# Kernel tuning notes

Hardware: AMD Instinct MI355X
Metric: run time of the kernel (lower is better)

The kernel has to match this reference:

```python
import jax, jax.numpy as jnp
import numpy as np

HEADS = 16
HEAD_DIM = 64
TOKEN_DIM = 1024
INNER = HEADS * HEAD_DIM


def setup_inputs() -> dict:
    key = jax.random.key(0)
    k1, k2, k3, k4 = jax.random.split(key, 4)
    x = jax.random.normal(k1, (2, 2048, TOKEN_DIM), dtype=jnp.float32)
    # nn.Linear(token_dim, inner*3, bias=False): weight [3*inner, token_dim]
    w_qkv = jax.random.normal(k2, (3 * INNER, TOKEN_DIM), dtype=jnp.float32) * (TOKEN_DIM ** -0.5)
    # nn.Linear(inner, token_dim): weight [token_dim, inner], bias [token_dim]
    w_out = jax.random.normal(k3, (TOKEN_DIM, INNER), dtype=jnp.float32) * (INNER ** -0.5)
    b_out = jax.random.normal(k4, (TOKEN_DIM,), dtype=jnp.float32) * 0.01
    return {"x": x, "w_qkv": w_qkv, "w_out": w_out, "b_out": b_out}


def reference(x, w_qkv, w_out, b_out):
    b, n, _ = x.shape
    scale = HEAD_DIM ** -0.5
    qkv = x @ w_qkv.T                                  # [b, n, 3*inner]
    q, k, v = jnp.split(qkv, 3, axis=-1)
    def split_heads(t):
        return t.reshape(b, n, HEADS, HEAD_DIM).transpose(0, 2, 1, 3)  # [b,h,n,d]
    q, k, v = split_heads(q), split_heads(k), split_heads(v)
    dot = jnp.einsum('bhtd,bhsd->bhts', q, k) * scale  # [b,h,n,n]
    attn = jax.nn.softmax(dot, axis=-1)
    out = jnp.einsum('bhts,bhsd->bhtd', attn, v)       # [b,h,n,d]
    out = out.transpose(0, 2, 1, 3).reshape(b, n, INNER)
    return out @ w_out.T + b_out
```

## Files before the change

kernel.cpp:

```cpp
#include <hip/hip_runtime.h>
#include <hip/hip_bf16.h>

typedef short short4v __attribute__((ext_vector_type(4)));
typedef short short8 __attribute__((ext_vector_type(8)));
typedef float float4v __attribute__((ext_vector_type(4)));

#define HEADS 16
#define HDIM 64
#define TOKDIM 1024
#define SEQ 2048
#define BATCH 2
#define BH (BATCH*HEADS)
#define MROWS (BATCH*SEQ)

__device__ __forceinline__ short f2b(float f) {
    __hip_bfloat16 h = __float2bfloat16(f);
    return *reinterpret_cast<short*>(&h);
}
__device__ __forceinline__ float b2f(short s) {
    __hip_bfloat16 h;
    *reinterpret_cast<short*>(&h) = s;
    return __bfloat162float(h);
}
__device__ __forceinline__ int pack2(float a, float b) {
    return (((int)f2b(b)) << 16) | (((int)f2b(a)) & 0xffff);
}

__device__ __forceinline__ short8 load8_f32_bf16(const float* __restrict__ p) {
    float4v a = *(const float4v*)p;
    float4v b = *(const float4v*)(p + 4);
    short8 r;
    r[0]=f2b(a[0]); r[1]=f2b(a[1]); r[2]=f2b(a[2]); r[3]=f2b(a[3]);
    r[4]=f2b(b[0]); r[5]=f2b(b[1]); r[6]=f2b(b[2]); r[7]=f2b(b[3]);
    return r;
}

#define BM 128
#define BN 128
#define BK 32
#define LDT 40

__global__ __launch_bounds__(256)
void gemm_qkv(const float* __restrict__ A, const float* __restrict__ W,
              short* __restrict__ Qo, short* __restrict__ Ko, short* __restrict__ Vto)
{
    __shared__ __align__(16) short As[BM*LDT];
    __shared__ __align__(16) short Bs[BN*LDT];
    const int tid  = threadIdx.x;
    const int lane = tid & 63;
    const int wave = tid >> 6;
    const int wm = wave >> 1, wn = wave & 1;
    const int m0 = blockIdx.x * BM;
    const int n0 = blockIdx.y * BN;
    const int col16 = lane & 15, quad = lane >> 4;
    const int Kdim = TOKDIM;

    float4v acc[4][4];
    #pragma unroll
    for (int i=0;i<4;i++)
        #pragma unroll
        for (int j=0;j<4;j++) acc[i][j] = (float4v){0.f,0.f,0.f,0.f};

    for (int k0 = 0; k0 < Kdim; k0 += BK) {
        __syncthreads();
        #pragma unroll
        for (int s = 0; s < 2; ++s) {
            int blk = tid + s*256;
            int r  = blk >> 2;
            int kb = blk & 3;
            *(short8*)&As[r*LDT + kb*8] = load8_f32_bf16(&A[(size_t)(m0 + r)*Kdim + k0 + kb*8]);
            *(short8*)&Bs[r*LDT + kb*8] = load8_f32_bf16(&W[(size_t)(n0 + r)*Kdim + k0 + kb*8]);
        }
        __syncthreads();
        short8 af[4], bfr[4];
        #pragma unroll
        for (int i=0;i<4;i++) af[i]  = *(const short8*)&As[(wm*64 + i*16 + col16)*LDT + quad*8];
        #pragma unroll
        for (int j=0;j<4;j++) bfr[j] = *(const short8*)&Bs[(wn*64 + j*16 + col16)*LDT + quad*8];
        #pragma unroll
        for (int i=0;i<4;i++)
            #pragma unroll
            for (int j=0;j<4;j++)
                acc[i][j] = __builtin_amdgcn_mfma_f32_16x16x32_bf16(af[i], bfr[j], acc[i][j], 0,0,0);
    }

    #pragma unroll
    for (int i=0;i<4;i++)
        #pragma unroll
        for (int j=0;j<4;j++) {
            const int n = n0 + wn*64 + j*16 + col16;
            const int part = n >> 10;
            const int h = (n & 1023) >> 6;
            const int d = n & 63;
            const int mb = m0 + wm*64 + i*16 + quad*4;
            const int b = mb >> 11;
            const int t = mb & 2047;
            if (part == 2) {
                union { short4v s; int2 i2; } w;
                #pragma unroll
                for (int r=0;r<4;r++) w.s[r] = f2b(acc[i][j][r]);
                *(int2*)&Vto[((size_t)(b*HEADS + h)*HDIM + d)*SEQ + t] = w.i2;
            } else {
                short* dst = (part == 0) ? Qo : Ko;
                #pragma unroll
                for (int r=0;r<4;r++)
                    dst[((size_t)(b*HEADS + h)*SEQ + t + r)*HDIM + d] = f2b(acc[i][j][r]);
            }
        }
}

__global__ __launch_bounds__(256)
void gemm_out(const short* __restrict__ A, const float* __restrict__ W,
              const float* __restrict__ bias, float* __restrict__ C)
{
    __shared__ __align__(16) short As[BM*LDT];
    __shared__ __align__(16) short Bs[BN*LDT];
    const int tid  = threadIdx.x;
    const int lane = tid & 63;
    const int wave = tid >> 6;
    const int wm = wave >> 1, wn = wave & 1;
    const int m0 = blockIdx.x * BM;
    const int n0 = blockIdx.y * BN;
    const int col16 = lane & 15, quad = lane >> 4;
    const int Kdim = TOKDIM, Ncols = TOKDIM;

    float4v acc[4][4];
    #pragma unroll
    for (int i=0;i<4;i++)
        #pragma unroll
        for (int j=0;j<4;j++) acc[i][j] = (float4v){0.f,0.f,0.f,0.f};

    for (int k0 = 0; k0 < Kdim; k0 += BK) {
        __syncthreads();
        #pragma unroll
        for (int s = 0; s < 2; ++s) {
            int blk = tid + s*256;
            int r  = blk >> 2;
            int kb = blk & 3;
            *(short8*)&As[r*LDT + kb*8] = *(const short8*)&A[(size_t)(m0 + r)*Kdim + k0 + kb*8];
            *(short8*)&Bs[r*LDT + kb*8] = load8_f32_bf16(&W[(size_t)(n0 + r)*Kdim + k0 + kb*8]);
        }
        __syncthreads();
        short8 af[4], bfr[4];
        #pragma unroll
        for (int i=0;i<4;i++) af[i]  = *(const short8*)&As[(wm*64 + i*16 + col16)*LDT + quad*8];
        #pragma unroll
        for (int j=0;j<4;j++) bfr[j] = *(const short8*)&Bs[(wn*64 + j*16 + col16)*LDT + quad*8];
        #pragma unroll
        for (int i=0;i<4;i++)
            #pragma unroll
            for (int j=0;j<4;j++)
                acc[i][j] = __builtin_amdgcn_mfma_f32_16x16x32_bf16(af[i], bfr[j], acc[i][j], 0,0,0);
    }

    #pragma unroll
    for (int i=0;i<4;i++)
        #pragma unroll
        for (int j=0;j<4;j++) {
            const int n = n0 + wn*64 + j*16 + col16;
            #pragma unroll
            for (int r=0;r<4;r++) {
                const int m = m0 + wm*64 + i*16 + quad*4 + r;
                C[(size_t)m*Ncols + n] = acc[i][j][r] + bias[n];
            }
        }
}

#define AQB 128
#define KT  64
#define VLD 72

__global__ __launch_bounds__(256, 4)
void attn_kernel(const short* __restrict__ Q, const short* __restrict__ K,
                 const short* __restrict__ Vt, short* __restrict__ AO)
{
    __shared__ __align__(16) short Ks[2][KT*VLD];
    __shared__ __align__(16) short Vs[2][HDIM*VLD];

    const int tid   = threadIdx.x;
    const int lane  = tid & 63;
    const int wave  = tid >> 6;
    const int col16 = lane & 15, quad = lane >> 4;
    const int bh = blockIdx.y;
    const int qb = blockIdx.x*AQB + wave*32;

    const short* Qb = Q  + (size_t)bh*SEQ*HDIM;
    const short* Kb = K  + (size_t)bh*SEQ*HDIM;
    const short* Vb = Vt + (size_t)bh*HDIM*SEQ;

    const int sr = tid >> 2;
    const int sc = (tid & 3) * 16;
    const int rho = sr & 31;
    const int kslot = (sr & 32) + ((rho & 4) << 2) + ((rho & 24) >> 1) + (rho & 3);

    short8 qf[2][2];
    #pragma unroll
    for (int qg=0; qg<2; ++qg)
        #pragma unroll
        for (int kh=0; kh<2; ++kh) {
            short8 raw = *(const short8*)&Qb[(size_t)(qb+qg*16+col16)*HDIM + kh*32 + quad*8];
            #pragma unroll
            for (int j=0;j<8;++j) raw[j] = f2b(b2f(raw[j]) * 0.125f);
            qf[qg][kh] = raw;
        }

    float4v o[2][4];
    #pragma unroll
    for (int qg=0;qg<2;qg++)
        #pragma unroll
        for (int dt=0;dt<4;dt++) o[qg][dt] = (float4v){0.f,0.f,0.f,0.f};
    float lsum[2] = {0.f, 0.f};

    {
        short8 k0 = *(const short8*)&Kb[(size_t)sr*HDIM + sc];
        short8 k1 = *(const short8*)&Kb[(size_t)sr*HDIM + sc + 8];
        short8 v0 = *(const short8*)&Vb[(size_t)sr*SEQ + sc];
        short8 v1 = *(const short8*)&Vb[(size_t)sr*SEQ + sc + 8];
        *(short8*)&Ks[0][kslot*VLD + sc]     = k0;
        *(short8*)&Ks[0][kslot*VLD + sc + 8] = k1;
        *(short8*)&Vs[0][sr*VLD + sc]        = v0;
        *(short8*)&Vs[0][sr*VLD + sc + 8]    = v1;
    }
    __syncthreads();

    const int NT = SEQ / KT;
    for (int tile = 0; tile < NT; ++tile) {
        const int buf = tile & 1;

        short8 nk0, nk1, nv0, nv1;
        const bool more = (tile + 1 < NT);
        if (more) {
            const int s1 = (tile + 1) * KT;
            nk0 = *(const short8*)&Kb[(size_t)(s1 + sr)*HDIM + sc];
            nk1 = *(const short8*)&Kb[(size_t)(s1 + sr)*HDIM + sc + 8];
            nv0 = *(const short8*)&Vb[(size_t)sr*SEQ + s1 + sc];
            nv1 = *(const short8*)&Vb[(size_t)sr*SEQ + s1 + sc + 8];
        }

        #pragma unroll
        for (int kk = 0; kk < 2; ++kk) {
            short8 ka[2][2];
            #pragma unroll
            for (int nt=0; nt<2; ++nt)
                #pragma unroll
                for (int kh=0; kh<2; ++kh)
                    ka[nt][kh] = *(const short8*)&Ks[buf][(kk*32 + nt*16 + col16)*VLD + kh*32 + quad*8];
            short8 va[4];
            #pragma unroll
            for (int dt=0; dt<4; ++dt)
                va[dt] = *(const short8*)&Vs[buf][(dt*16 + col16)*VLD + kk*32 + quad*8];

            #pragma unroll
            for (int qg=0; qg<2; ++qg) {
                float4v st[2];
                #pragma unroll
                for (int nt=0; nt<2; ++nt) {
                    float4v z = (float4v){0.f,0.f,0.f,0.f};
                    z = __builtin_amdgcn_mfma_f32_16x16x32_bf16(ka[nt][0], qf[qg][0], z, 0,0,0);
                    z = __builtin_amdgcn_mfma_f32_16x16x32_bf16(ka[nt][1], qf[qg][1], z, 0,0,0);
                    st[nt] = z;
                }
                union { int i[4]; short8 s8; } pb;
                float p00 = __expf(st[0][0]), p01 = __expf(st[0][1]);
                float p02 = __expf(st[0][2]), p03 = __expf(st[0][3]);
                float p10 = __expf(st[1][0]), p11 = __expf(st[1][1]);
                float p12 = __expf(st[1][2]), p13 = __expf(st[1][3]);
                lsum[qg] += ((p00+p01) + (p02+p03)) + ((p10+p11) + (p12+p13));
                pb.i[0] = pack2(p00, p01); pb.i[1] = pack2(p02, p03);
                pb.i[2] = pack2(p10, p11); pb.i[3] = pack2(p12, p13);

                #pragma unroll
                for (int dt=0; dt<4; ++dt)
                    o[qg][dt] = __builtin_amdgcn_mfma_f32_16x16x32_bf16(va[dt], pb.s8, o[qg][dt], 0,0,0);
            }
        }

        if (more) {
            const int nb = buf ^ 1;
            *(short8*)&Ks[nb][kslot*VLD + sc]     = nk0;
            *(short8*)&Ks[nb][kslot*VLD + sc + 8] = nk1;
            *(short8*)&Vs[nb][sr*VLD + sc]        = nv0;
            *(short8*)&Vs[nb][sr*VLD + sc + 8]    = nv1;
        }
        __syncthreads();
    }

    #pragma unroll
    for (int qg=0; qg<2; ++qg) {
        lsum[qg] += __shfl_xor(lsum[qg], 16);
        lsum[qg] += __shfl_xor(lsum[qg], 32);
    }

    const int b = bh >> 4, h = bh & 15;
    #pragma unroll
    for (int qg=0; qg<2; ++qg) {
        const float inv = 1.0f / lsum[qg];
        const int t = qb + qg*16 + col16;
        #pragma unroll
        for (int dt=0; dt<4; ++dt) {
            union { short4v s; int2 i2; } w;
            #pragma unroll
            for (int r=0;r<4;++r) w.s[r] = f2b(o[qg][dt][r] * inv);
            *(int2*)&AO[((size_t)(b*SEQ + t))*TOKDIM + h*64 + dt*16 + quad*4] = w.i2;
        }
    }
}

extern "C" void kernel_launch(void* const* d_in, const int* in_sizes, int n_in,
                              void* d_out, int out_size, void* d_ws, size_t ws_size,
                              hipStream_t stream)
{
    const float* x    = (const float*)d_in[0];
    const float* wqkv = (const float*)d_in[1];
    const float* wout = (const float*)d_in[2];
    const float* bout = (const float*)d_in[3];
    float* out = (float*)d_out;

    char* ws = (char*)d_ws;
    const size_t SZ = (size_t)BH*SEQ*HDIM*sizeof(short);
    short* Qt = (short*)(ws);
    short* Kt = (short*)(ws + SZ);
    short* AO = (short*)(ws + 2*SZ);
    short* Vt = (short*)(ws + 3*SZ);

    gemm_qkv<<<dim3(MROWS/BM, (3*TOKDIM)/BN), 256, 0, stream>>>(x, wqkv, Qt, Kt, Vt);
    attn_kernel<<<dim3(SEQ/AQB, BH), 256, 0, stream>>>(Qt, Kt, Vt, AO);
    gemm_out<<<dim3(MROWS/BM, TOKDIM/BN), 256, 0, stream>>>(AO, wout, bout, out);
}
```

Baseline: 201.3 us.

## Pre-convert inputs to bf16 and stage GEMM tiles via direct global-to-LDS loads

Adds a conversion kernel that turns x, w_qkv and w_out into bf16 once per call. The QKV and output GEMMs can then stage tiles with global_load_lds straight into unpadded shared memory, instead of each block re-reading and converting fp32 tiles through registers. The output GEMM tile is reduced to 64 rows, which doubles its block count, and the bias load is hoisted out of the store loop. The trade-off is an extra launch and extra memory traffic for the conversion, plus possible LDS bank conflicts because the padding was removed.

```diff
diff --git a/kernel.cpp b/kernel.cpp
--- a/kernel.cpp
+++ b/kernel.cpp
@@ -25,7 +25,6 @@
 __device__ __forceinline__ int pack2(float a, float b) {
     return (((int)f2b(b)) << 16) | (((int)f2b(a)) & 0xffff);
 }
-
 __device__ __forceinline__ short8 load8_f32_bf16(const float* __restrict__ p) {
     float4v a = *(const float4v*)p;
     float4v b = *(const float4v*)(p + 4);
@@ -35,25 +34,42 @@
     return r;
 }
 
-#define BM 128
-#define BN 128
-#define BK 32
-#define LDT 40
+__device__ __forceinline__ void stage16(const void* g, void* l) {
+    __builtin_amdgcn_global_load_lds((const __attribute__((address_space(1))) void*)g,
+                                     (__attribute__((address_space(3))) void*)l, 16, 0, 0);
+}
 
 __global__ __launch_bounds__(256)
-void gemm_qkv(const float* __restrict__ A, const float* __restrict__ W,
+void cvt_bf16(const float* __restrict__ x,  short* __restrict__ xb,  int n8x,
+              const float* __restrict__ wq, short* __restrict__ wqb, int n8q,
+              const float* __restrict__ wo, short* __restrict__ wob, int n8o)
+{
+    int i = blockIdx.x*256 + threadIdx.x;
+    const float* s; short* d; int off;
+    if (i < n8x)                  { s = x;  d = xb;  off = i; }
+    else if (i < n8x + n8q)       { s = wq; d = wqb; off = i - n8x; }
+    else if (i < n8x + n8q + n8o) { s = wo; d = wob; off = i - n8x - n8q; }
+    else return;
+    *(short8*)&d[(size_t)off*8] = load8_f32_bf16(&s[(size_t)off*8]);
+}
+
+template<int ABF16>
+__global__ __launch_bounds__(256)
+void gemm_qkv(const void* __restrict__ Ap, const short* __restrict__ Wq,
               short* __restrict__ Qo, short* __restrict__ Ko, short* __restrict__ Vto)
 {
-    __shared__ __align__(16) short As[BM*LDT];
-    __shared__ __align__(16) short Bs[BN*LDT];
+    __shared__ __align__(16) short As[128*32];
+    __shared__ __align__(16) short Bs[128*32];
     const int tid  = threadIdx.x;
     const int lane = tid & 63;
     const int wave = tid >> 6;
     const int wm = wave >> 1, wn = wave & 1;
-    const int m0 = blockIdx.x * BM;
-    const int n0 = blockIdx.y * BN;
+    const int m0 = blockIdx.x * 128;
+    const int n0 = blockIdx.y * 128;
     const int col16 = lane & 15, quad = lane >> 4;
-    const int Kdim = TOKDIM;
+
+    const int srow = lane >> 2;
+    const int scol = (lane & 3) * 8;
 
     float4v acc[4][4];
     #pragma unroll
@@ -61,22 +77,36 @@
         #pragma unroll
         for (int j=0;j<4;j++) acc[i][j] = (float4v){0.f,0.f,0.f,0.f};
 
-    for (int k0 = 0; k0 < Kdim; k0 += BK) {
-        __syncthreads();
-        #pragma unroll
-        for (int s = 0; s < 2; ++s) {
-            int blk = tid + s*256;
-            int r  = blk >> 2;
-            int kb = blk & 3;
-            *(short8*)&As[r*LDT + kb*8] = load8_f32_bf16(&A[(size_t)(m0 + r)*Kdim + k0 + kb*8]);
-            *(short8*)&Bs[r*LDT + kb*8] = load8_f32_bf16(&W[(size_t)(n0 + r)*Kdim + k0 + kb*8]);
-        }
-        __syncthreads();
+    for (int k0 = 0; k0 < TOKDIM; k0 += 32) {
+        __syncthreads();
+        if (ABF16) {
+            const short* A = (const short*)Ap;
+            #pragma unroll
+            for (int j=0;j<2;++j) {
+                const int rb = (wave*2 + j) * 16;
+                stage16(&A[(size_t)(m0 + rb + srow)*TOKDIM + k0 + scol], &As[rb*32]);
+            }
+        } else {
+            const float* A = (const float*)Ap;
+            #pragma unroll
+            for (int s=0;s<2;++s) {
+                int blk = tid + s*256;
+                int r = blk >> 2, kb = blk & 3;
+                *(short8*)&As[r*32 + kb*8] = load8_f32_bf16(&A[(size_t)(m0+r)*TOKDIM + k0 + kb*8]);
+            }
+        }
+        #pragma unroll
+        for (int j=0;j<2;++j) {
+            const int rb = (wave*2 + j) * 16;
+            stage16(&Wq[(size_t)(n0 + rb + srow)*TOKDIM + k0 + scol], &Bs[rb*32]);
+        }
+        __syncthreads();
+
         short8 af[4], bfr[4];
         #pragma unroll
-        for (int i=0;i<4;i++) af[i]  = *(const short8*)&As[(wm*64 + i*16 + col16)*LDT + quad*8];
-        #pragma unroll
-        for (int j=0;j<4;j++) bfr[j] = *(const short8*)&Bs[(wn*64 + j*16 + col16)*LDT + quad*8];
+        for (int i=0;i<4;i++) af[i]  = *(const short8*)&As[(wm*64 + i*16 + col16)*32 + quad*8];
+        #pragma unroll
+        for (int j=0;j<4;j++) bfr[j] = *(const short8*)&Bs[(wn*64 + j*16 + col16)*32 + quad*8];
         #pragma unroll
         for (int i=0;i<4;i++)
             #pragma unroll
@@ -110,58 +140,63 @@
 }
 
 __global__ __launch_bounds__(256)
-void gemm_out(const short* __restrict__ A, const float* __restrict__ W,
+void gemm_out(const short* __restrict__ A, const short* __restrict__ W,
               const float* __restrict__ bias, float* __restrict__ C)
 {
-    __shared__ __align__(16) short As[BM*LDT];
-    __shared__ __align__(16) short Bs[BN*LDT];
+    __shared__ __align__(16) short As[64*32];
+    __shared__ __align__(16) short Bs[128*32];
     const int tid  = threadIdx.x;
     const int lane = tid & 63;
     const int wave = tid >> 6;
     const int wm = wave >> 1, wn = wave & 1;
-    const int m0 = blockIdx.x * BM;
-    const int n0 = blockIdx.y * BN;
+    const int m0 = blockIdx.x * 64;
+    const int n0 = blockIdx.y * 128;
     const int col16 = lane & 15, quad = lane >> 4;
-    const int Kdim = TOKDIM, Ncols = TOKDIM;
-
-    float4v acc[4][4];
-    #pragma unroll
-    for (int i=0;i<4;i++)
+
+    const int srow = lane >> 2;
+    const int scol = (lane & 3) * 8;
+
+    float4v acc[2][4];
+    #pragma unroll
+    for (int i=0;i<2;i++)
         #pragma unroll
         for (int j=0;j<4;j++) acc[i][j] = (float4v){0.f,0.f,0.f,0.f};
 
-    for (int k0 = 0; k0 < Kdim; k0 += BK) {
-        __syncthreads();
-        #pragma unroll
-        for (int s = 0; s < 2; ++s) {
-            int blk = tid + s*256;
-            int r  = blk >> 2;
-            int kb = blk & 3;
-            *(short8*)&As[r*LDT + kb*8] = *(const short8*)&A[(size_t)(m0 + r)*Kdim + k0 + kb*8];
-            *(short8*)&Bs[r*LDT + kb*8] = load8_f32_bf16(&W[(size_t)(n0 + r)*Kdim + k0 + kb*8]);
-        }
-        __syncthreads();
-        short8 af[4], bfr[4];
-        #pragma unroll
-        for (int i=0;i<4;i++) af[i]  = *(const short8*)&As[(wm*64 + i*16 + col16)*LDT + quad*8];
-        #pragma unroll
-        for (int j=0;j<4;j++) bfr[j] = *(const short8*)&Bs[(wn*64 + j*16 + col16)*LDT + quad*8];
-        #pragma unroll
-        for (int i=0;i<4;i++)
+    for (int k0 = 0; k0 < TOKDIM; k0 += 32) {
+        __syncthreads();
+        {
+            const int rb = wave * 16;
+            stage16(&A[(size_t)(m0 + rb + srow)*TOKDIM + k0 + scol], &As[rb*32]);
+        }
+        #pragma unroll
+        for (int j=0;j<2;++j) {
+            const int rb = (wave*2 + j) * 16;
+            stage16(&W[(size_t)(n0 + rb + srow)*TOKDIM + k0 + scol], &Bs[rb*32]);
+        }
+        __syncthreads();
+
+        short8 af[2], bfr[4];
+        #pragma unroll
+        for (int i=0;i<2;i++) af[i]  = *(const short8*)&As[(wm*32 + i*16 + col16)*32 + quad*8];
+        #pragma unroll
+        for (int j=0;j<4;j++) bfr[j] = *(const short8*)&Bs[(wn*64 + j*16 + col16)*32 + quad*8];
+        #pragma unroll
+        for (int i=0;i<2;i++)
             #pragma unroll
             for (int j=0;j<4;j++)
                 acc[i][j] = __builtin_amdgcn_mfma_f32_16x16x32_bf16(af[i], bfr[j], acc[i][j], 0,0,0);
     }
 
     #pragma unroll
-    for (int i=0;i<4;i++)
+    for (int i=0;i<2;i++)
         #pragma unroll
         for (int j=0;j<4;j++) {
             const int n = n0 + wn*64 + j*16 + col16;
+            const float bn = bias[n];
             #pragma unroll
             for (int r=0;r<4;r++) {
-                const int m = m0 + wm*64 + i*16 + quad*4 + r;
-                C[(size_t)m*Ncols + n] = acc[i][j][r] + bias[n];
+                const int m = m0 + wm*32 + i*16 + quad*4 + r;
+                C[(size_t)m*TOKDIM + n] = acc[i][j][r] + bn;
             }
         }
 }
@@ -317,13 +352,45 @@
     float* out = (float*)d_out;
 
     char* ws = (char*)d_ws;
-    const size_t SZ = (size_t)BH*SEQ*HDIM*sizeof(short);
-    short* Qt = (short*)(ws);
-    short* Kt = (short*)(ws + SZ);
-    short* AO = (short*)(ws + 2*SZ);
-    short* Vt = (short*)(ws + 3*SZ);
-
-    gemm_qkv<<<dim3(MROWS/BM, (3*TOKDIM)/BN), 256, 0, stream>>>(x, wqkv, Qt, Kt, Vt);
+    const size_t SZ   = (size_t)BH*SEQ*HDIM*sizeof(short);
+    const size_t WQB  = (size_t)3*TOKDIM*TOKDIM*sizeof(short);
+    const size_t WOB  = (size_t)TOKDIM*TOKDIM*sizeof(short);
+    const size_t NEED_FULL = SZ + WQB + WOB + 3*SZ;
+    const bool full = ws_size >= NEED_FULL;
+
+    short *Xb, *Wqb, *Wob, *Qt, *Kt, *Vt, *AO;
+    if (full) {
+        Xb  = (short*)ws;
+        Wqb = (short*)(ws + SZ);
+        Wob = (short*)(ws + SZ + WQB);
+        Qt  = (short*)(ws + SZ + WQB + WOB);
+        Kt  = Qt + SZ/2;
+        Vt  = Kt + SZ/2;
+        AO  = Xb;
+    } else {
+        Xb  = nullptr;
+        Wqb = (short*)ws;
+        Wob = (short*)(ws + WQB);
+        Qt  = (short*)(ws + WQB + WOB);
+        Kt  = Qt + SZ/2;
+        Vt  = Kt + SZ/2;
+        AO  = Vt + SZ/2;
+    }
+
+    const int n8x = full ? (BATCH*SEQ*TOKDIM)/8 : 0;
+    const int n8q = (3*TOKDIM*TOKDIM)/8;
+    const int n8o = (TOKDIM*TOKDIM)/8;
+    const int cvt_blocks = (n8x + n8q + n8o + 255) / 256;
+    cvt_bf16<<<cvt_blocks, 256, 0, stream>>>(x, Xb, n8x, wqkv, Wqb, n8q, wout, Wob, n8o);
+
+    if (full)
+        gemm_qkv<1><<<dim3(MROWS/128, (3*TOKDIM)/128), 256, 0, stream>>>(
+            (const void*)Xb, Wqb, Qt, Kt, Vt);
+    else
+        gemm_qkv<0><<<dim3(MROWS/128, (3*TOKDIM)/128), 256, 0, stream>>>(
+            (const void*)x, Wqb, Qt, Kt, Vt);
+
     attn_kernel<<<dim3(SEQ/AQB, BH), 256, 0, stream>>>(Qt, Kt, Vt, AO);
-    gemm_out<<<dim3(MROWS/BM, TOKDIM/BN), 256, 0, stream>>>(AO, wout, bout, out);
-}
+
+    gemm_out<<<dim3(MROWS/64, TOKDIM/128), 256, 0, stream>>>(AO, Wob, bout, out);
+}
```

Measured after the change: 181.2 us. 1.11x faster.
